# Kernel optimization log

Hardware: AMD Instinct MI355X
Metric: run time of the kernel (lower is better)

The kernel has to match this reference:

```python
import jax, jax.numpy as jnp
import numpy as np

D = 32      # input_size
H = 256     # hidden_size
B = 4096    # batch
EPS = 1e-12

def _masks(order="A"):
    # Standard MADE degree-based masks. order 'A' = natural ordering.
    deg_in = np.arange(1, D + 1) if order == "A" else np.arange(D, 0, -1)
    deg_h = (np.arange(H) % (D - 1)) + 1
    m0 = (deg_h[None, :] >= deg_in[:, None]).astype(np.float32)  # [D,H] input->hidden
    m1 = (deg_h[None, :] >= deg_h[:, None]).astype(np.float32)   # [H,H] hidden->hidden
    m2 = (deg_in[None, :] > deg_h[:, None]).astype(np.float32)   # [H,D] hidden->output (strict)
    return jnp.asarray(m0), jnp.asarray(m1), jnp.asarray(m2)

M0, M1, M2 = _masks()

def _made(y, W0, b0, W1, b1, W2, b2):
    # masked MLP: D -> H -> H -> D (num_hiddens=2 hidden layers)
    h = jax.nn.relu(y @ (W0 * M0) + b0)
    h = jax.nn.relu(h @ (W1 * M1) + b1)
    return h @ (W2 * M2) + b2

def setup_inputs() -> dict:
    key = jax.random.key(0)
    ks = jax.random.split(key, 8)
    def w(k, fi, fo):
        return jax.random.normal(k, (fi, fo), jnp.float32) / np.sqrt(fi)
    inp = {"x": jax.random.normal(ks[0], (B, D), jnp.float32)}
    i = 1
    for n in ("mu", "lv"):
        inp[n + "_W0"] = w(ks[i], D, H); inp[n + "_b0"] = jnp.zeros((H,), jnp.float32); i += 1
        inp[n + "_W1"] = w(ks[i], H, H); inp[n + "_b1"] = jnp.zeros((H,), jnp.float32); i += 1
        inp[n + "_W2"] = w(ks[i], H, D); inp[n + "_b2"] = jnp.zeros((D,), jnp.float32); i += 1
    return inp

def reference(x, mu_W0, mu_b0, mu_W1, mu_b1, mu_W2, mu_b2,
              lv_W0, lv_b0, lv_W1, lv_b1, lv_W2, lv_b2):
    # AFMADEBlock.forward: D sequential fixed-point iterations of the
    def step(carry, _):
        y, _ls = carry
        mu = _made(y, mu_W0, mu_b0, mu_W1, mu_b1, mu_W2, mu_b2)
        logstd = _made(y, lv_W0, lv_b0, lv_W1, lv_b1, lv_W2, lv_b2) * 0.5
        y_new = (x - mu) / (jnp.exp(logstd) + EPS)
        return (y_new, logstd), None
    init = (jnp.zeros_like(x), jnp.zeros_like(x))
    (y, logstd), _ = jax.lax.scan(step, init, None, length=D)
    return y, logstd.sum(axis=1)
```

## Files before the change

kernel.cpp:

```cpp
#include <hip/hip_runtime.h>

#define DD   32
#define HH   256
#define BB   4096
#define RR   2
#define EPSF 1e-12f

__device__ __forceinline__ int made_pi(int p) {
    return (p < 72) ? (p / 9) + 31 * (p % 9)
                    : (8 + (p - 72) / 8) + 31 * ((p - 72) % 8);
}
__device__ __forceinline__ int made_off(int d) {
    return (d <= 9) ? 9 * (d - 1) : 8 * d;
}

#define NW0   (DD * HH)
#define NW1   (HH * HH)
#define NETF  (NW0 + NW1 + HH + HH)
#define W2IOFF (2 * NETF)
#define NW2I  (HH * 64)
#define WSNEED ((size_t)(W2IOFF + NW2I) * 4)

__global__ void made_prep(
    const float* __restrict__ muW0, const float* __restrict__ mub0,
    const float* __restrict__ muW1, const float* __restrict__ mub1,
    const float* __restrict__ muW2,
    const float* __restrict__ lvW0, const float* __restrict__ lvb0,
    const float* __restrict__ lvW1, const float* __restrict__ lvb1,
    const float* __restrict__ lvW2,
    float* __restrict__ ws)
{
    const int t = threadIdx.x;
    const int b = blockIdx.x;
    __shared__ float rowbuf[HH];

    if (b < 512) {
        const int n = b >> 8, p = b & 255;
        const int h = made_pi(p);
        const float* W1 = n ? lvW1 : muW1;
        float* o = ws + (size_t)n * NETF;
        *reinterpret_cast<float4*>(&rowbuf[4 * t]) =
            *reinterpret_cast<const float4*>(W1 + h * HH + 4 * t);
        __syncthreads();
        float4 w;
        w.x = rowbuf[made_pi(4 * t + 0)];
        w.y = rowbuf[made_pi(4 * t + 1)];
        w.z = rowbuf[made_pi(4 * t + 2)];
        w.w = rowbuf[made_pi(4 * t + 3)];
        *reinterpret_cast<float4*>(o + NW0 + p * HH + 4 * t) = w;
        if (t == 0) {
            o[NW0 + NW1 + p]      = (n ? lvb0 : mub0)[h];
            o[NW0 + NW1 + HH + p] = (n ? lvb1 : mub1)[h];
        }
    } else if (b < 768) {
        const int p = b - 512;
        const int h = made_pi(p);
        const int n = t >> 5, dd = t & 31;
        ws[W2IOFF + p * 64 + t] = (n ? lvW2 : muW2)[h * DD + dd];
    } else {
        const int idx = b - 768;
        const int n = idx >> 5, i = idx & 31;
        const float* W0 = n ? lvW0 : muW0;
        float* o = ws + (size_t)n * NETF;
        *reinterpret_cast<float4*>(&rowbuf[4 * t]) =
            *reinterpret_cast<const float4*>(W0 + i * HH + 4 * t);
        __syncthreads();
        float4 w;
        w.x = rowbuf[made_pi(4 * t + 0)];
        w.y = rowbuf[made_pi(4 * t + 1)];
        w.z = rowbuf[made_pi(4 * t + 2)];
        w.w = rowbuf[made_pi(4 * t + 3)];
        *reinterpret_cast<float4*>(o + i * HH + 4 * t) = w;
    }
}

__global__ __launch_bounds__(256, 2) void made_main(
    const float* __restrict__ ws, const float* __restrict__ x,
    const float* __restrict__ mub2, const float* __restrict__ lvb2,
    float* __restrict__ out)
{
    const int lane = threadIdx.x & 63;
    const int wv   = threadIdx.x >> 6;
    const int row0 = ((blockIdx.x << 2) + wv) * RR;
    const int c4   = lane << 2;
    const int nn   = lane >> 5;
    const int ddl  = lane & 31;

    const float* W0p[2] = {ws,       ws + NETF};
    const float* W1p[2] = {ws + NW0, ws + NETF + NW0};
    const float* W2i    = ws + W2IOFF;

    float h0[2][4][RR], h1[2][4][RR];
    #pragma unroll
    for (int n = 0; n < 2; ++n) {
        const float* bb = ws + (size_t)n * NETF + NW0 + NW1;
        const float4 v0 = *reinterpret_cast<const float4*>(bb + c4);
        const float4 v1 = *reinterpret_cast<const float4*>(bb + HH + c4);
        const float a0[4] = {v0.x, v0.y, v0.z, v0.w};
        const float a1[4] = {v1.x, v1.y, v1.z, v1.w};
        #pragma unroll
        for (int s = 0; s < 4; ++s)
            #pragma unroll
            for (int r = 0; r < RR; ++r) { h0[n][s][r] = a0[s]; h1[n][s][r] = a1[s]; }
    }

    const float accinit = nn ? lvb2[ddl] : mub2[ddl];
    float acc[RR];
    #pragma unroll
    for (int r = 0; r < RR; ++r) acc[r] = accinit;

    float xvr[RR];
    #pragma unroll
    for (int r = 0; r < RR; ++r) xvr[r] = x[(row0 + r) * DD + ddl];

    __shared__ float A[4][2][RR][12];
    __shared__ float Bf[4][2][RR][12];

    float yprev[RR], lsum[RR], ysave[RR];
    #pragma unroll
    for (int r = 0; r < RR; ++r) { lsum[r] = 0.f; ysave[r] = 0.f; }

    #pragma unroll
    for (int r = 0; r < RR; ++r) {
        const float mu  = __shfl(acc[r], 0, 64);
        const float lv  = __shfl(acc[r], 32, 64);
        const float ls2 = 0.5f * lv;
        lsum[r] += ls2;
        const float yd = (__shfl(xvr[r], 0, 64) - mu) / (__expf(ls2) + EPSF);
        yprev[r] = yd;
        if (lane == 0) ysave[r] = yd;
    }

    for (int d = 1; d < DD; ++d) {
        const int off = made_off(d);
        const int nk  = (d <= 8) ? 9 : 8;
        int r8 = off + 8; if (r8 > 255) r8 = 255;

        const float4 w0m = *reinterpret_cast<const float4*>(W0p[0] + (d - 1) * HH + c4);
        const float4 w0l = *reinterpret_cast<const float4*>(W0p[1] + (d - 1) * HH + c4);
        float4 w1m[9], w1l[9];
        {
            const float* a = W1p[0] + off * HH + c4;
            const float* b = W1p[1] + off * HH + c4;
            #pragma unroll
            for (int k = 0; k < 8; ++k) {
                w1m[k] = *reinterpret_cast<const float4*>(a + k * HH);
                w1l[k] = *reinterpret_cast<const float4*>(b + k * HH);
            }
            w1m[8] = *reinterpret_cast<const float4*>(W1p[0] + r8 * HH + c4);
            w1l[8] = *reinterpret_cast<const float4*>(W1p[1] + r8 * HH + c4);
        }
        float w2[9];
        {
            const float* w2c = W2i + off * 64 + lane;
            #pragma unroll
            for (int k = 0; k < 8; ++k) w2[k] = w2c[k * 64];
            w2[8] = W2i[r8 * 64 + lane];
        }

        #pragma unroll
        for (int r = 0; r < RR; ++r) {
            h0[0][0][r] = fmaf(yprev[r], w0m.x, h0[0][0][r]);
            h0[0][1][r] = fmaf(yprev[r], w0m.y, h0[0][1][r]);
            h0[0][2][r] = fmaf(yprev[r], w0m.z, h0[0][2][r]);
            h0[0][3][r] = fmaf(yprev[r], w0m.w, h0[0][3][r]);
            h0[1][0][r] = fmaf(yprev[r], w0l.x, h0[1][0][r]);
            h0[1][1][r] = fmaf(yprev[r], w0l.y, h0[1][1][r]);
            h0[1][2][r] = fmaf(yprev[r], w0l.z, h0[1][2][r]);
            h0[1][3][r] = fmaf(yprev[r], w0l.w, h0[1][3][r]);
        }

        if (d >= 9 && lane == 0) {
            #pragma unroll
            for (int n = 0; n < 2; ++n)
                #pragma unroll
                for (int r = 0; r < RR; ++r) {
                    A[wv][n][r][8]  = 0.f;
                    Bf[wv][n][r][8] = 0.f;
                }
        }
        #pragma unroll
        for (int s = 0; s < 4; ++s) {
            const int k = c4 + s - off;
            if ((unsigned)k < (unsigned)nk) {
                #pragma unroll
                for (int r = 0; r < RR; ++r) {
                    A[wv][0][r][k] = fmaxf(h0[0][s][r], 0.f);
                    A[wv][1][r][k] = fmaxf(h0[1][s][r], 0.f);
                }
            }
        }
        float av[2][RR][9];
        #pragma unroll
        for (int n = 0; n < 2; ++n)
            #pragma unroll
            for (int r = 0; r < RR; ++r) {
                const float4 a03 = *reinterpret_cast<const float4*>(&A[wv][n][r][0]);
                const float4 a47 = *reinterpret_cast<const float4*>(&A[wv][n][r][4]);
                av[n][r][0] = a03.x; av[n][r][1] = a03.y;
                av[n][r][2] = a03.z; av[n][r][3] = a03.w;
                av[n][r][4] = a47.x; av[n][r][5] = a47.y;
                av[n][r][6] = a47.z; av[n][r][7] = a47.w;
                av[n][r][8] = A[wv][n][r][8];
            }

        #pragma unroll
        for (int k = 0; k < 9; ++k) {
            #pragma unroll
            for (int r = 0; r < RR; ++r) {
                h1[0][0][r] = fmaf(av[0][r][k], w1m[k].x, h1[0][0][r]);
                h1[0][1][r] = fmaf(av[0][r][k], w1m[k].y, h1[0][1][r]);
                h1[0][2][r] = fmaf(av[0][r][k], w1m[k].z, h1[0][2][r]);
                h1[0][3][r] = fmaf(av[0][r][k], w1m[k].w, h1[0][3][r]);
                h1[1][0][r] = fmaf(av[1][r][k], w1l[k].x, h1[1][0][r]);
                h1[1][1][r] = fmaf(av[1][r][k], w1l[k].y, h1[1][1][r]);
                h1[1][2][r] = fmaf(av[1][r][k], w1l[k].z, h1[1][2][r]);
                h1[1][3][r] = fmaf(av[1][r][k], w1l[k].w, h1[1][3][r]);
            }
        }

        #pragma unroll
        for (int s = 0; s < 4; ++s) {
            const int k = c4 + s - off;
            if ((unsigned)k < (unsigned)nk) {
                #pragma unroll
                for (int r = 0; r < RR; ++r) {
                    Bf[wv][0][r][k] = fmaxf(h1[0][s][r], 0.f);
                    Bf[wv][1][r][k] = fmaxf(h1[1][s][r], 0.f);
                }
            }
        }
        float rb[RR][9];
        #pragma unroll
        for (int r = 0; r < RR; ++r) {
            const float4 b03 = *reinterpret_cast<const float4*>(&Bf[wv][nn][r][0]);
            const float4 b47 = *reinterpret_cast<const float4*>(&Bf[wv][nn][r][4]);
            rb[r][0] = b03.x; rb[r][1] = b03.y; rb[r][2] = b03.z; rb[r][3] = b03.w;
            rb[r][4] = b47.x; rb[r][5] = b47.y; rb[r][6] = b47.z; rb[r][7] = b47.w;
            rb[r][8] = Bf[wv][nn][r][8];
        }
        #pragma unroll
        for (int k = 0; k < 9; ++k)
            #pragma unroll
            for (int r = 0; r < RR; ++r)
                acc[r] = fmaf(rb[r][k], w2[k], acc[r]);

        #pragma unroll
        for (int r = 0; r < RR; ++r) {
            const float mu  = __shfl(acc[r], d, 64);
            const float lv  = __shfl(acc[r], 32 + d, 64);
            const float ls2 = 0.5f * lv;
            lsum[r] += ls2;
            const float yd = (__shfl(xvr[r], d, 64) - mu) / (__expf(ls2) + EPSF);
            yprev[r] = yd;
            if (lane == d) ysave[r] = yd;
        }
    }

    #pragma unroll
    for (int r = 0; r < RR; ++r) {
        if (lane < DD) out[(row0 + r) * DD + lane] = ysave[r];
        if (lane == 0) out[BB * DD + row0 + r] = lsum[r];
    }
}

__global__ __launch_bounds__(64, 1) void made_inv_fb(
    const float* __restrict__ x,
    const float* __restrict__ muW0, const float* __restrict__ mub0,
    const float* __restrict__ muW1, const float* __restrict__ mub1,
    const float* __restrict__ muW2, const float* __restrict__ mub2,
    const float* __restrict__ lvW0, const float* __restrict__ lvb0,
    const float* __restrict__ lvW1, const float* __restrict__ lvb1,
    const float* __restrict__ lvW2, const float* __restrict__ lvb2,
    float* __restrict__ out)
{
    const int lane    = threadIdx.x;
    const int rowBase = blockIdx.x * 4;
    const int hb      = lane << 2;
    int deg[4];
    #pragma unroll
    for (int s = 0; s < 4; ++s) deg[s] = ((hb + s) % 31) + 1;
    const float* Wp0[2] = {muW0, lvW0};
    const float* Bp0[2] = {mub0, lvb0};
    const float* Wp1[2] = {muW1, lvW1};
    const float* Bp1[2] = {mub1, lvb1};
    const float* Wp2[2] = {muW2, lvW2};
    float h0pre[2][4][4], h1pre[2][4][4], r1[2][4][4], yprev[4], lsum[4];
    #pragma unroll
    for (int n = 0; n < 2; ++n) {
        const float4 b0v = *reinterpret_cast<const float4*>(Bp0[n] + hb);
        const float4 b1v = *reinterpret_cast<const float4*>(Bp1[n] + hb);
        const float b0a[4] = {b0v.x, b0v.y, b0v.z, b0v.w};
        const float b1a[4] = {b1v.x, b1v.y, b1v.z, b1v.w};
        #pragma unroll
        for (int s = 0; s < 4; ++s)
            #pragma unroll
            for (int r = 0; r < 4; ++r) {
                h0pre[n][s][r] = b0a[s]; h1pre[n][s][r] = b1a[s]; r1[n][s][r] = 0.f;
            }
    }
    #pragma unroll
    for (int r = 0; r < 4; ++r) { yprev[r] = 0.f; lsum[r] = 0.f; }
    __shared__ float lds_a[2][4][12];
    for (int d = 0; d < DD; ++d) {
        if (d >= 1) {
            #pragma unroll
            for (int n = 0; n < 2; ++n) {
                const float4 w0 = *reinterpret_cast<const float4*>(Wp0[n] + (d - 1) * HH + hb);
                const float w0a[4] = {w0.x, w0.y, w0.z, w0.w};
                #pragma unroll
                for (int s = 0; s < 4; ++s)
                    #pragma unroll
                    for (int r = 0; r < 4; ++r)
                        h0pre[n][s][r] = fmaf(yprev[r], w0a[s], h0pre[n][s][r]);
            }
            #pragma unroll
            for (int n = 0; n < 2; ++n)
                #pragma unroll
                for (int s = 0; s < 4; ++s)
                    if (deg[s] == d) {
                        const int k = (hb + s - (d - 1)) / 31;
                        #pragma unroll
                        for (int r = 0; r < 4; ++r)
                            lds_a[n][r][k] = fmaxf(h0pre[n][s][r], 0.f);
                    }
            __syncthreads();
            const bool nine = (d <= 8);
            #pragma unroll
            for (int n = 0; n < 2; ++n) {
                const float* W1r = Wp1[n] + (size_t)(d - 1) * HH + hb;
                float4 w1v[9];
                #pragma unroll
                for (int k = 0; k < 8; ++k)
                    w1v[k] = *reinterpret_cast<const float4*>(W1r + k * 31 * HH);
                if (nine) w1v[8] = *reinterpret_cast<const float4*>(W1r + 8 * 31 * HH);
                #pragma unroll
                for (int r = 0; r < 4; ++r) {
                    const float4 a03 = *reinterpret_cast<const float4*>(&lds_a[n][r][0]);
                    const float4 a47 = *reinterpret_cast<const float4*>(&lds_a[n][r][4]);
                    const float av[8] = {a03.x, a03.y, a03.z, a03.w, a47.x, a47.y, a47.z, a47.w};
                    #pragma unroll
                    for (int k = 0; k < 8; ++k) {
                        const float wk[4] = {w1v[k].x, w1v[k].y, w1v[k].z, w1v[k].w};
                        #pragma unroll
                        for (int s = 0; s < 4; ++s)
                            h1pre[n][s][r] = fmaf(av[k], wk[s], h1pre[n][s][r]);
                    }
                    if (nine) {
                        const float a8 = lds_a[n][r][8];
                        const float wk[4] = {w1v[8].x, w1v[8].y, w1v[8].z, w1v[8].w};
                        #pragma unroll
                        for (int s = 0; s < 4; ++s)
                            h1pre[n][s][r] = fmaf(a8, wk[s], h1pre[n][s][r]);
                    }
                }
            }
            #pragma unroll
            for (int n = 0; n < 2; ++n)
                #pragma unroll
                for (int s = 0; s < 4; ++s)
                    if (deg[s] == d)
                        #pragma unroll
                        for (int r = 0; r < 4; ++r)
                            r1[n][s][r] = fmaxf(h1pre[n][s][r], 0.f);
            __syncthreads();
        }
        float w2v[2][4];
        #pragma unroll
        for (int n = 0; n < 2; ++n)
            #pragma unroll
            for (int s = 0; s < 4; ++s)
                w2v[n][s] = Wp2[n][(hb + s) * DD + d];
        float red[2][4];
        #pragma unroll
        for (int n = 0; n < 2; ++n)
            #pragma unroll
            for (int r = 0; r < 4; ++r) {
                float p = 0.f;
                #pragma unroll
                for (int s = 0; s < 4; ++s) p = fmaf(r1[n][s][r], w2v[n][s], p);
                red[n][r] = p;
            }
        #pragma unroll
        for (int m = 1; m < 64; m <<= 1)
            #pragma unroll
            for (int n = 0; n < 2; ++n)
                #pragma unroll
                for (int r = 0; r < 4; ++r)
                    red[n][r] += __shfl_xor(red[n][r], m, 64);
        const float b2m = mub2[d], b2l = lvb2[d];
        #pragma unroll
        for (int r = 0; r < 4; ++r) {
            const float mu = red[0][r] + b2m;
            const float logstd = 0.5f * (red[1][r] + b2l);
            lsum[r] += logstd;
            const float yd = (x[(rowBase + r) * DD + d] - mu) / (__expf(logstd) + EPSF);
            yprev[r] = yd;
            if (lane == 0) out[(rowBase + r) * DD + d] = yd;
        }
    }
    if (lane == 0)
        #pragma unroll
        for (int r = 0; r < 4; ++r) out[BB * DD + rowBase + r] = lsum[r];
}

extern "C" void kernel_launch(void* const* d_in, const int* in_sizes, int n_in,
                              void* d_out, int out_size, void* d_ws, size_t ws_size,
                              hipStream_t stream) {
    const float* x    = (const float*)d_in[0];
    const float* muW0 = (const float*)d_in[1];
    const float* mub0 = (const float*)d_in[2];
    const float* muW1 = (const float*)d_in[3];
    const float* mub1 = (const float*)d_in[4];
    const float* muW2 = (const float*)d_in[5];
    const float* mub2 = (const float*)d_in[6];
    const float* lvW0 = (const float*)d_in[7];
    const float* lvb0 = (const float*)d_in[8];
    const float* lvW1 = (const float*)d_in[9];
    const float* lvb1 = (const float*)d_in[10];
    const float* lvW2 = (const float*)d_in[11];
    const float* lvb2 = (const float*)d_in[12];
    float* out = (float*)d_out;

    if (ws_size >= WSNEED) {
        float* ws = (float*)d_ws;
        made_prep<<<dim3(832), dim3(64), 0, stream>>>(
            muW0, mub0, muW1, mub1, muW2,
            lvW0, lvb0, lvW1, lvb1, lvW2, ws);
        made_main<<<dim3(BB / (4 * RR)), dim3(256), 0, stream>>>(ws, x, mub2, lvb2, out);
    } else {
        made_inv_fb<<<dim3(BB / 4), dim3(64), 0, stream>>>(x,
            muW0, mub0, muW1, mub1, muW2, mub2,
            lvW0, lvb0, lvW1, lvb1, lvW2, lvb2, out);
    }
}
```

Baseline: 136.3 us.

## Replace LDS staging of hidden activations with wave readlane broadcasts

The per-step exchange of newly valid hidden units moves out of shared memory (write, then read back) and into scalar readlane broadcasts from the owning lanes. The loop is split into two templated phases so that steps 9 and up use aligned 8-row windows with no masking. The first 8 steps use a 12-row window with predicated zeroing. The output layer is restructured so each lane keeps separate mu and logvar accumulators, and W2 is interleaved into float2 pairs. This removes LDS round trips and their waits. In exchange, the first phase does extra FMA work, readlane calls are serialized, and the added accumulators raise register pressure.

```diff
diff --git a/kernel.cpp b/kernel.cpp
--- a/kernel.cpp
+++ b/kernel.cpp
@@ -10,8 +10,9 @@
     return (p < 72) ? (p / 9) + 31 * (p % 9)
                     : (8 + (p - 72) / 8) + 31 * ((p - 72) % 8);
 }
-__device__ __forceinline__ int made_off(int d) {
-    return (d <= 9) ? 9 * (d - 1) : 8 * d;
+
+__device__ __forceinline__ float rlf(float v, int srclane) {
+    return __int_as_float(__builtin_amdgcn_readlane(__float_as_int(v), srclane));
 }
 
 #define NW0   (DD * HH)
@@ -56,7 +57,7 @@
         const int p = b - 512;
         const int h = made_pi(p);
         const int n = t >> 5, dd = t & 31;
-        ws[W2IOFF + p * 64 + t] = (n ? lvW2 : muW2)[h * DD + dd];
+        ws[W2IOFF + p * 64 + dd * 2 + n] = (n ? lvW2 : muW2)[h * DD + dd];
     } else {
         const int idx = b - 768;
         const int n = idx >> 5, i = idx & 31;
@@ -74,6 +75,109 @@
     }
 }
 
+template <int W, bool MASK>
+__device__ __forceinline__ void made_step(
+    const int d, const int off, const int base, const int L0,
+    const int c4, const int lane, const int ddl,
+    const float* __restrict__ W0m, const float* __restrict__ W0l,
+    const float* __restrict__ W1m, const float* __restrict__ W1l,
+    const float* __restrict__ W2i,
+    float (&h0)[2][4][RR], float (&h1)[2][4][RR],
+    float (&accm)[RR], float (&accl)[RR],
+    float (&yprev)[RR], float (&lsum)[RR], float (&ysave)[RR],
+    const float (&xvr)[RR])
+{
+    const float4 w0m = *reinterpret_cast<const float4*>(W0m + (d - 1) * HH + c4);
+    const float4 w0l = *reinterpret_cast<const float4*>(W0l + (d - 1) * HH + c4);
+    float4 w1m[W], w1l[W];
+    #pragma unroll
+    for (int m = 0; m < W; ++m) {
+        w1m[m] = *reinterpret_cast<const float4*>(W1m + (base + m) * HH + c4);
+        w1l[m] = *reinterpret_cast<const float4*>(W1l + (base + m) * HH + c4);
+    }
+    float2 w2v[W];
+    #pragma unroll
+    for (int m = 0; m < W; ++m)
+        w2v[m] = *reinterpret_cast<const float2*>(W2i + (base + m) * 64 + 2 * ddl);
+
+    #pragma unroll
+    for (int r = 0; r < RR; ++r) {
+        h0[0][0][r] = fmaf(yprev[r], w0m.x, h0[0][0][r]);
+        h0[0][1][r] = fmaf(yprev[r], w0m.y, h0[0][1][r]);
+        h0[0][2][r] = fmaf(yprev[r], w0m.z, h0[0][2][r]);
+        h0[0][3][r] = fmaf(yprev[r], w0m.w, h0[0][3][r]);
+        h0[1][0][r] = fmaf(yprev[r], w0l.x, h0[1][0][r]);
+        h0[1][1][r] = fmaf(yprev[r], w0l.y, h0[1][1][r]);
+        h0[1][2][r] = fmaf(yprev[r], w0l.z, h0[1][2][r]);
+        h0[1][3][r] = fmaf(yprev[r], w0l.w, h0[1][3][r]);
+    }
+
+    float a0[2][4][RR];
+    #pragma unroll
+    for (int s = 0; s < 4; ++s) {
+        const bool ing = !MASK || ((unsigned)(c4 + s - off) < 9u);
+        #pragma unroll
+        for (int n = 0; n < 2; ++n)
+            #pragma unroll
+            for (int r = 0; r < RR; ++r)
+                a0[n][s][r] = ing ? fmaxf(h0[n][s][r], 0.f) : 0.f;
+    }
+
+    #pragma unroll
+    for (int m = 0; m < W; ++m) {
+        const int sl = L0 + (m >> 2);
+        float avm[RR], avl[RR];
+        #pragma unroll
+        for (int r = 0; r < RR; ++r) {
+            avm[r] = rlf(a0[0][m & 3][r], sl);
+            avl[r] = rlf(a0[1][m & 3][r], sl);
+        }
+        #pragma unroll
+        for (int r = 0; r < RR; ++r) {
+            h1[0][0][r] = fmaf(avm[r], w1m[m].x, h1[0][0][r]);
+            h1[0][1][r] = fmaf(avm[r], w1m[m].y, h1[0][1][r]);
+            h1[0][2][r] = fmaf(avm[r], w1m[m].z, h1[0][2][r]);
+            h1[0][3][r] = fmaf(avm[r], w1m[m].w, h1[0][3][r]);
+            h1[1][0][r] = fmaf(avl[r], w1l[m].x, h1[1][0][r]);
+            h1[1][1][r] = fmaf(avl[r], w1l[m].y, h1[1][1][r]);
+            h1[1][2][r] = fmaf(avl[r], w1l[m].z, h1[1][2][r]);
+            h1[1][3][r] = fmaf(avl[r], w1l[m].w, h1[1][3][r]);
+        }
+    }
+
+    float b1[2][4][RR];
+    #pragma unroll
+    for (int s = 0; s < 4; ++s) {
+        const bool ing = !MASK || ((unsigned)(c4 + s - off) < 9u);
+        #pragma unroll
+        for (int n = 0; n < 2; ++n)
+            #pragma unroll
+            for (int r = 0; r < RR; ++r)
+                b1[n][s][r] = ing ? fmaxf(h1[n][s][r], 0.f) : 0.f;
+    }
+
+    #pragma unroll
+    for (int m = 0; m < W; ++m) {
+        const int sl = L0 + (m >> 2);
+        #pragma unroll
+        for (int r = 0; r < RR; ++r) {
+            accm[r] = fmaf(rlf(b1[0][m & 3][r], sl), w2v[m].x, accm[r]);
+            accl[r] = fmaf(rlf(b1[1][m & 3][r], sl), w2v[m].y, accl[r]);
+        }
+    }
+
+    #pragma unroll
+    for (int r = 0; r < RR; ++r) {
+        const float mu  = rlf(accm[r], d);
+        const float lv  = rlf(accl[r], d);
+        const float ls2 = 0.5f * lv;
+        lsum[r] += ls2;
+        const float yd = (rlf(xvr[r], d) - mu) / (__expf(ls2) + EPSF);
+        yprev[r] = yd;
+        if (lane == d) ysave[r] = yd;
+    }
+}
+
 __global__ __launch_bounds__(256, 2) void made_main(
     const float* __restrict__ ws, const float* __restrict__ x,
     const float* __restrict__ mub2, const float* __restrict__ lvb2,
@@ -83,12 +187,13 @@
     const int wv   = threadIdx.x >> 6;
     const int row0 = ((blockIdx.x << 2) + wv) * RR;
     const int c4   = lane << 2;
-    const int nn   = lane >> 5;
     const int ddl  = lane & 31;
 
-    const float* W0p[2] = {ws,       ws + NETF};
-    const float* W1p[2] = {ws + NW0, ws + NETF + NW0};
-    const float* W2i    = ws + W2IOFF;
+    const float* W0m = ws;
+    const float* W0l = ws + NETF;
+    const float* W1m = ws + NW0;
+    const float* W1l = ws + NETF + NW0;
+    const float* W2i = ws + W2IOFF;
 
     float h0[2][4][RR], h1[2][4][RR];
     #pragma unroll
@@ -96,165 +201,54 @@
         const float* bb = ws + (size_t)n * NETF + NW0 + NW1;
         const float4 v0 = *reinterpret_cast<const float4*>(bb + c4);
         const float4 v1 = *reinterpret_cast<const float4*>(bb + HH + c4);
-        const float a0[4] = {v0.x, v0.y, v0.z, v0.w};
-        const float a1[4] = {v1.x, v1.y, v1.z, v1.w};
+        const float a0i[4] = {v0.x, v0.y, v0.z, v0.w};
+        const float a1i[4] = {v1.x, v1.y, v1.z, v1.w};
         #pragma unroll
         for (int s = 0; s < 4; ++s)
             #pragma unroll
-            for (int r = 0; r < RR; ++r) { h0[n][s][r] = a0[s]; h1[n][s][r] = a1[s]; }
-    }
-
-    const float accinit = nn ? lvb2[ddl] : mub2[ddl];
-    float acc[RR];
-    #pragma unroll
-    for (int r = 0; r < RR; ++r) acc[r] = accinit;
+            for (int r = 0; r < RR; ++r) { h0[n][s][r] = a0i[s]; h1[n][s][r] = a1i[s]; }
+    }
+
+    float accm[RR], accl[RR];
+    {
+        const float bm = mub2[ddl], bl = lvb2[ddl];
+        #pragma unroll
+        for (int r = 0; r < RR; ++r) { accm[r] = bm; accl[r] = bl; }
+    }
 
     float xvr[RR];
     #pragma unroll
     for (int r = 0; r < RR; ++r) xvr[r] = x[(row0 + r) * DD + ddl];
 
-    __shared__ float A[4][2][RR][12];
-    __shared__ float Bf[4][2][RR][12];
-
     float yprev[RR], lsum[RR], ysave[RR];
     #pragma unroll
     for (int r = 0; r < RR; ++r) { lsum[r] = 0.f; ysave[r] = 0.f; }
 
     #pragma unroll
     for (int r = 0; r < RR; ++r) {
-        const float mu  = __shfl(acc[r], 0, 64);
-        const float lv  = __shfl(acc[r], 32, 64);
+        const float mu  = rlf(accm[r], 0);
+        const float lv  = rlf(accl[r], 0);
         const float ls2 = 0.5f * lv;
         lsum[r] += ls2;
-        const float yd = (__shfl(xvr[r], 0, 64) - mu) / (__expf(ls2) + EPSF);
+        const float yd = (rlf(xvr[r], 0) - mu) / (__expf(ls2) + EPSF);
         yprev[r] = yd;
         if (lane == 0) ysave[r] = yd;
     }
 
-    for (int d = 1; d < DD; ++d) {
-        const int off = made_off(d);
-        const int nk  = (d <= 8) ? 9 : 8;
-        int r8 = off + 8; if (r8 > 255) r8 = 255;
-
-        const float4 w0m = *reinterpret_cast<const float4*>(W0p[0] + (d - 1) * HH + c4);
-        const float4 w0l = *reinterpret_cast<const float4*>(W0p[1] + (d - 1) * HH + c4);
-        float4 w1m[9], w1l[9];
-        {
-            const float* a = W1p[0] + off * HH + c4;
-            const float* b = W1p[1] + off * HH + c4;
-            #pragma unroll
-            for (int k = 0; k < 8; ++k) {
-                w1m[k] = *reinterpret_cast<const float4*>(a + k * HH);
-                w1l[k] = *reinterpret_cast<const float4*>(b + k * HH);
-            }
-            w1m[8] = *reinterpret_cast<const float4*>(W1p[0] + r8 * HH + c4);
-            w1l[8] = *reinterpret_cast<const float4*>(W1p[1] + r8 * HH + c4);
-        }
-        float w2[9];
-        {
-            const float* w2c = W2i + off * 64 + lane;
-            #pragma unroll
-            for (int k = 0; k < 8; ++k) w2[k] = w2c[k * 64];
-            w2[8] = W2i[r8 * 64 + lane];
-        }
-
-        #pragma unroll
-        for (int r = 0; r < RR; ++r) {
-            h0[0][0][r] = fmaf(yprev[r], w0m.x, h0[0][0][r]);
-            h0[0][1][r] = fmaf(yprev[r], w0m.y, h0[0][1][r]);
-            h0[0][2][r] = fmaf(yprev[r], w0m.z, h0[0][2][r]);
-            h0[0][3][r] = fmaf(yprev[r], w0m.w, h0[0][3][r]);
-            h0[1][0][r] = fmaf(yprev[r], w0l.x, h0[1][0][r]);
-            h0[1][1][r] = fmaf(yprev[r], w0l.y, h0[1][1][r]);
-            h0[1][2][r] = fmaf(yprev[r], w0l.z, h0[1][2][r]);
-            h0[1][3][r] = fmaf(yprev[r], w0l.w, h0[1][3][r]);
-        }
-
-        if (d >= 9 && lane == 0) {
-            #pragma unroll
-            for (int n = 0; n < 2; ++n)
-                #pragma unroll
-                for (int r = 0; r < RR; ++r) {
-                    A[wv][n][r][8]  = 0.f;
-                    Bf[wv][n][r][8] = 0.f;
-                }
-        }
-        #pragma unroll
-        for (int s = 0; s < 4; ++s) {
-            const int k = c4 + s - off;
-            if ((unsigned)k < (unsigned)nk) {
-                #pragma unroll
-                for (int r = 0; r < RR; ++r) {
-                    A[wv][0][r][k] = fmaxf(h0[0][s][r], 0.f);
-                    A[wv][1][r][k] = fmaxf(h0[1][s][r], 0.f);
-                }
-            }
-        }
-        float av[2][RR][9];
-        #pragma unroll
-        for (int n = 0; n < 2; ++n)
-            #pragma unroll
-            for (int r = 0; r < RR; ++r) {
-                const float4 a03 = *reinterpret_cast<const float4*>(&A[wv][n][r][0]);
-                const float4 a47 = *reinterpret_cast<const float4*>(&A[wv][n][r][4]);
-                av[n][r][0] = a03.x; av[n][r][1] = a03.y;
-                av[n][r][2] = a03.z; av[n][r][3] = a03.w;
-                av[n][r][4] = a47.x; av[n][r][5] = a47.y;
-                av[n][r][6] = a47.z; av[n][r][7] = a47.w;
-                av[n][r][8] = A[wv][n][r][8];
-            }
-
-        #pragma unroll
-        for (int k = 0; k < 9; ++k) {
-            #pragma unroll
-            for (int r = 0; r < RR; ++r) {
-                h1[0][0][r] = fmaf(av[0][r][k], w1m[k].x, h1[0][0][r]);
-                h1[0][1][r] = fmaf(av[0][r][k], w1m[k].y, h1[0][1][r]);
-                h1[0][2][r] = fmaf(av[0][r][k], w1m[k].z, h1[0][2][r]);
-                h1[0][3][r] = fmaf(av[0][r][k], w1m[k].w, h1[0][3][r]);
-                h1[1][0][r] = fmaf(av[1][r][k], w1l[k].x, h1[1][0][r]);
-                h1[1][1][r] = fmaf(av[1][r][k], w1l[k].y, h1[1][1][r]);
-                h1[1][2][r] = fmaf(av[1][r][k], w1l[k].z, h1[1][2][r]);
-                h1[1][3][r] = fmaf(av[1][r][k], w1l[k].w, h1[1][3][r]);
-            }
-        }
-
-        #pragma unroll
-        for (int s = 0; s < 4; ++s) {
-            const int k = c4 + s - off;
-            if ((unsigned)k < (unsigned)nk) {
-                #pragma unroll
-                for (int r = 0; r < RR; ++r) {
-                    Bf[wv][0][r][k] = fmaxf(h1[0][s][r], 0.f);
-                    Bf[wv][1][r][k] = fmaxf(h1[1][s][r], 0.f);
-                }
-            }
-        }
-        float rb[RR][9];
-        #pragma unroll
-        for (int r = 0; r < RR; ++r) {
-            const float4 b03 = *reinterpret_cast<const float4*>(&Bf[wv][nn][r][0]);
-            const float4 b47 = *reinterpret_cast<const float4*>(&Bf[wv][nn][r][4]);
-            rb[r][0] = b03.x; rb[r][1] = b03.y; rb[r][2] = b03.z; rb[r][3] = b03.w;
-            rb[r][4] = b47.x; rb[r][5] = b47.y; rb[r][6] = b47.z; rb[r][7] = b47.w;
-            rb[r][8] = Bf[wv][nn][r][8];
-        }
-        #pragma unroll
-        for (int k = 0; k < 9; ++k)
-            #pragma unroll
-            for (int r = 0; r < RR; ++r)
-                acc[r] = fmaf(rb[r][k], w2[k], acc[r]);
-
-        #pragma unroll
-        for (int r = 0; r < RR; ++r) {
-            const float mu  = __shfl(acc[r], d, 64);
-            const float lv  = __shfl(acc[r], 32 + d, 64);
-            const float ls2 = 0.5f * lv;
-            lsum[r] += ls2;
-            const float yd = (__shfl(xvr[r], d, 64) - mu) / (__expf(ls2) + EPSF);
-            yprev[r] = yd;
-            if (lane == d) ysave[r] = yd;
-        }
+    #pragma unroll 1
+    for (int d = 1; d <= 8; ++d) {
+        const int off  = 9 * (d - 1);
+        const int base = off & ~3;
+        made_step<12, true>(d, off, base, base >> 2, c4, lane, ddl,
+                            W0m, W0l, W1m, W1l, W2i,
+                            h0, h1, accm, accl, yprev, lsum, ysave, xvr);
+    }
+    #pragma unroll 1
+    for (int d = 9; d < DD; ++d) {
+        const int off = 8 * d;
+        made_step<8, false>(d, off, off, off >> 2, c4, lane, ddl,
+                            W0m, W0l, W1m, W1l, W2i,
+                            h0, h1, accm, accl, yprev, lsum, ysave, xvr);
     }
 
     #pragma unroll
```

New measurement: 148.6 us. 1.09x slower.

## Double-buffer per-step weight slices in LDS with register prefetch

Applied to the files above, without the earlier changes.

Each step's W0 row, nine W1 rows for both networks and the W2 slice are now staged into a double-buffered shared-memory area. The next step's slice is loaded into registers early in the current step and written to the other buffer at the end, followed by a block barrier. The aim is to have the four waves of a block share one global fetch of the weights and to hide global latency behind compute. In exchange it adds about 45 KB of LDS per block, which may limit occupancy, plus extra registers for the staging buffer and one __syncthreads per step.

```diff
diff --git a/kernel.cpp b/kernel.cpp
--- a/kernel.cpp
+++ b/kernel.cpp
@@ -20,6 +20,13 @@
 #define W2IOFF (2 * NETF)
 #define NW2I  (HH * 64)
 #define WSNEED ((size_t)(W2IOFF + NW2I) * 4)
+
+#define LW1L  2304
+#define LW0M  4608
+#define LW0L  4864
+#define LW2   5120
+#define LDSZ  5696
+#define NSTG  1424
 
 __global__ void made_prep(
     const float* __restrict__ muW0, const float* __restrict__ mub0,
@@ -74,21 +81,66 @@
     }
 }
 
+__device__ __forceinline__ const float4* stage_src(
+    int i, int dn,
+    const float* __restrict__ W1m, const float* __restrict__ W1l,
+    const float* __restrict__ W0m, const float* __restrict__ W0l,
+    const float* __restrict__ W2i)
+{
+    const int offn = made_off(dn);
+    if (i < 1152) {
+        const int net = i >= 576;
+        const int ii  = net ? i - 576 : i;
+        const int row9 = ii >> 6, c4i = ii & 63;
+        int grow = offn + row9; if (grow > 255) grow = 255;
+        const float* W1 = net ? W1l : W1m;
+        return reinterpret_cast<const float4*>(W1 + grow * HH + 4 * c4i);
+    } else if (i < 1280) {
+        const int j = i - 1152, net = j >> 6, c4i = j & 63;
+        const float* W0 = net ? W0l : W0m;
+        return reinterpret_cast<const float4*>(W0 + (dn - 1) * HH + 4 * c4i);
+    } else {
+        const int j = i - 1280, row9 = j >> 4, c4i = j & 15;
+        int grow = offn + row9; if (grow > 255) grow = 255;
+        return reinterpret_cast<const float4*>(W2i + grow * 64 + 4 * c4i);
+    }
+}
+__device__ __forceinline__ int stage_dst(int i) {
+    if (i < 1152) {
+        const int net = i >= 576;
+        const int ii  = net ? i - 576 : i;
+        return net * LW1L + (ii >> 6) * 256 + 4 * (ii & 63);
+    } else if (i < 1280) {
+        const int j = i - 1152;
+        return LW0M + (j >> 6) * 256 + 4 * (j & 63);
+    } else {
+        const int j = i - 1280;
+        return LW2 + (j >> 4) * 64 + 4 * (j & 15);
+    }
+}
+
 __global__ __launch_bounds__(256, 2) void made_main(
     const float* __restrict__ ws, const float* __restrict__ x,
     const float* __restrict__ mub2, const float* __restrict__ lvb2,
     float* __restrict__ out)
 {
-    const int lane = threadIdx.x & 63;
-    const int wv   = threadIdx.x >> 6;
+    const int t    = threadIdx.x;
+    const int lane = t & 63;
+    const int wv   = t >> 6;
     const int row0 = ((blockIdx.x << 2) + wv) * RR;
     const int c4   = lane << 2;
     const int nn   = lane >> 5;
     const int ddl  = lane & 31;
 
-    const float* W0p[2] = {ws,       ws + NETF};
-    const float* W1p[2] = {ws + NW0, ws + NETF + NW0};
-    const float* W2i    = ws + W2IOFF;
+    const float* W1m = ws + NW0;
+    const float* W1l = ws + NETF + NW0;
+    const float* W0m = ws;
+    const float* W0l = ws + NETF;
+    const float* W2i = ws + W2IOFF;
+
+    __shared__ float WB[2][LDSZ];
+    __shared__ float A[4][2][RR][12];
+    __shared__ float Bf[4][2][RR][12];
 
     float h0[2][4][RR], h1[2][4][RR];
     #pragma unroll
@@ -113,12 +165,16 @@
     #pragma unroll
     for (int r = 0; r < RR; ++r) xvr[r] = x[(row0 + r) * DD + ddl];
 
-    __shared__ float A[4][2][RR][12];
-    __shared__ float Bf[4][2][RR][12];
-
     float yprev[RR], lsum[RR], ysave[RR];
     #pragma unroll
     for (int r = 0; r < RR; ++r) { lsum[r] = 0.f; ysave[r] = 0.f; }
+
+    float4 st[6];
+    #pragma unroll
+    for (int it = 0; it < 6; ++it) {
+        const int i = t + it * 256;
+        if (i < NSTG) st[it] = *stage_src(i, 1, W1m, W1l, W0m, W0l, W2i);
+    }
 
     #pragma unroll
     for (int r = 0; r < RR; ++r) {
@@ -131,32 +187,36 @@
         if (lane == 0) ysave[r] = yd;
     }
 
+    #pragma unroll
+    for (int it = 0; it < 6; ++it) {
+        const int i = t + it * 256;
+        if (i < NSTG) *reinterpret_cast<float4*>(&WB[1][stage_dst(i)]) = st[it];
+    }
+    __syncthreads();
+
     for (int d = 1; d < DD; ++d) {
         const int off = made_off(d);
         const int nk  = (d <= 8) ? 9 : 8;
-        int r8 = off + 8; if (r8 > 255) r8 = 255;
-
-        const float4 w0m = *reinterpret_cast<const float4*>(W0p[0] + (d - 1) * HH + c4);
-        const float4 w0l = *reinterpret_cast<const float4*>(W0p[1] + (d - 1) * HH + c4);
+        const float* wb = &WB[d & 1][0];
+        const int nst = (d < DD - 1) ? NSTG : 0;
+
+        #pragma unroll
+        for (int it = 0; it < 6; ++it) {
+            const int i = t + it * 256;
+            if (i < nst) st[it] = *stage_src(i, d + 1, W1m, W1l, W0m, W0l, W2i);
+        }
+
+        const float4 w0m = *reinterpret_cast<const float4*>(wb + LW0M + c4);
+        const float4 w0l = *reinterpret_cast<const float4*>(wb + LW0L + c4);
         float4 w1m[9], w1l[9];
-        {
-            const float* a = W1p[0] + off * HH + c4;
-            const float* b = W1p[1] + off * HH + c4;
-            #pragma unroll
-            for (int k = 0; k < 8; ++k) {
-                w1m[k] = *reinterpret_cast<const float4*>(a + k * HH);
-                w1l[k] = *reinterpret_cast<const float4*>(b + k * HH);
-            }
-            w1m[8] = *reinterpret_cast<const float4*>(W1p[0] + r8 * HH + c4);
-            w1l[8] = *reinterpret_cast<const float4*>(W1p[1] + r8 * HH + c4);
+        #pragma unroll
+        for (int k = 0; k < 9; ++k) {
+            w1m[k] = *reinterpret_cast<const float4*>(wb + k * HH + c4);
+            w1l[k] = *reinterpret_cast<const float4*>(wb + LW1L + k * HH + c4);
         }
         float w2[9];
-        {
-            const float* w2c = W2i + off * 64 + lane;
-            #pragma unroll
-            for (int k = 0; k < 8; ++k) w2[k] = w2c[k * 64];
-            w2[8] = W2i[r8 * 64 + lane];
-        }
+        #pragma unroll
+        for (int k = 0; k < 9; ++k) w2[k] = wb[LW2 + k * 64 + lane];
 
         #pragma unroll
         for (int r = 0; r < RR; ++r) {
@@ -255,6 +315,13 @@
             yprev[r] = yd;
             if (lane == d) ysave[r] = yd;
         }
+
+        #pragma unroll
+        for (int it = 0; it < 6; ++it) {
+            const int i = t + it * 256;
+            if (i < nst) *reinterpret_cast<float4*>(&WB[(d + 1) & 1][stage_dst(i)]) = st[it];
+        }
+        __syncthreads();
     }
 
     #pragma unroll
```

Result: slower. 204.0 us (+49.7%).
